# Kernel tuning notes

Measured on AMD Instinct MI355X. Metric: run time of the kernel, lower is better.

## Reference

```python
import jax, jax.numpy as jnp
import numpy as np

N_NODES = 100000


def gcn_conv(x, edge_index, edge_weight, W, b):
    """PyG GCNConv (normalize=True, add_self_loops=True): lin -> gcn_norm -> scatter-add -> +bias."""
    n = x.shape[0]
    src, dst = edge_index[0], edge_index[1]
    # add self-loops with fill_value=1
    loop = jnp.arange(n, dtype=edge_index.dtype)
    src = jnp.concatenate([src, loop])
    dst = jnp.concatenate([dst, loop])
    ew = jnp.concatenate([edge_weight, jnp.ones((n,), dtype=x.dtype)])
    # symmetric normalization: deg computed at target (col)
    deg = jax.ops.segment_sum(ew, dst, num_segments=n)
    dinv = jnp.where(deg > 0, jax.lax.rsqrt(deg), 0.0).astype(x.dtype)
    norm = dinv[src] * ew * dinv[dst]  # [E+N]
    xl = x @ W  # [N, out]
    msg = norm[:, None] * xl[src]  # gather + scale
    out = jax.ops.segment_sum(msg, dst, num_segments=n)  # scatter-add at target
    return out + b


def setup_inputs() -> dict:
    key = jax.random.key(0)
    ks = jax.random.split(key, 8)
    n, e = N_NODES, 1600000
    c_in, c_hid, c_out = 40, 64, 40
    x = jax.random.normal(ks[0], (n, c_in), dtype=jnp.float32)
    edge_index = jax.random.randint(ks[1], (2, e), 0, n, dtype=jnp.int64)
    edge_weight = jax.random.uniform(ks[2], (e,), dtype=jnp.float32)
    s1 = 1.0 / np.sqrt(c_in)
    s2 = 1.0 / np.sqrt(c_hid)
    W1 = jax.random.uniform(ks[3], (c_in, c_hid), dtype=jnp.float32, minval=-s1, maxval=s1)
    b1 = jnp.zeros((c_hid,), dtype=jnp.float32)
    W2 = jax.random.uniform(ks[4], (c_hid, c_out), dtype=jnp.float32, minval=-s2, maxval=s2)
    b2 = jnp.zeros((c_out,), dtype=jnp.float32)
    return {"x": x, "edge_index": edge_index, "edge_weight": edge_weight,
            "W1": W1, "b1": b1, "W2": W2, "b2": b2}


def reference(x, edge_index, edge_weight, W1, b1, W2, b2):
    # eval mode: dropout is identity
    h = gcn_conv(x, edge_index, edge_weight, W1, b1)
    h = jax.nn.relu(h)
    out = gcn_conv(h, edge_index, edge_weight, W2, b2)
    return out
```

## Files before the change

### kernel.cpp

```cpp
#include <hip/hip_runtime.h>
#include <hip/hip_fp16.h>

#define FIX 33554432.0f
#define FIXINV (1.0f / 33554432.0f)

typedef unsigned long long ull;

#define EB 1024
#define CSH 9
#define CNODES 512
#define MAXNB 256

__global__ void zero_small_k(int* p, int total) {
    int i = blockIdx.x * blockDim.x + threadIdx.x;
    if (i < total) p[i] = 0;
}

__global__ void bcount_k(const int* __restrict__ dst, int* __restrict__ bcnt, int e, int NB) {
    __shared__ int lh[MAXNB];
    for (int i = threadIdx.x; i < NB; i += blockDim.x) lh[i] = 0;
    __syncthreads();
    int cls = blockIdx.x & 7;
    int base = blockIdx.x * EB + threadIdx.x * 4;
    if (base + 3 < e) {
        int4 d4 = *reinterpret_cast<const int4*>(dst + base);
        atomicAdd(&lh[d4.x >> CSH], 1);
        atomicAdd(&lh[d4.y >> CSH], 1);
        atomicAdd(&lh[d4.z >> CSH], 1);
        atomicAdd(&lh[d4.w >> CSH], 1);
    } else {
        for (int i = base; i < e && i < base + 4; ++i) atomicAdd(&lh[dst[i] >> CSH], 1);
    }
    __syncthreads();
    for (int i = threadIdx.x; i < NB; i += blockDim.x) {
        int c = lh[i];
        if (c) atomicAdd(&bcnt[(i * 8 + cls) * 16], c);
    }
}

__global__ void bscan_k(const int* __restrict__ bcnt, int* __restrict__ bbase,
                        int* __restrict__ gcur, int M, int NB, int e) {
    __shared__ int lds[256];
    int per = (M + 255) / 256;
    int tid = threadIdx.x;
    int s = 0;
    for (int j = 0; j < per; ++j) {
        int idx = tid * per + j;
        if (idx < M) s += bcnt[idx * 16];
    }
    lds[tid] = s;
    __syncthreads();
    for (int off = 1; off < 256; off <<= 1) {
        int v = (tid >= off) ? lds[tid - off] : 0;
        __syncthreads();
        lds[tid] += v;
        __syncthreads();
    }
    int run = lds[tid] - s;
    for (int j = 0; j < per; ++j) {
        int idx = tid * per + j;
        if (idx < M) {
            gcur[idx * 16] = run;
            if ((idx & 7) == 0) bbase[idx >> 3] = run;
            run += bcnt[idx * 16];
        }
    }
    if (tid == 0) bbase[NB] = e;
}

__global__ void part1_k(const int* __restrict__ src, const int* __restrict__ dst,
                        const float* __restrict__ ew, int* gcur, ull* __restrict__ tmp,
                        int e, int NB) {
    __shared__ int lh[MAXNB];
    __shared__ int lb[MAXNB];
    for (int i = threadIdx.x; i < NB; i += blockDim.x) lh[i] = 0;
    __syncthreads();
    int cls = blockIdx.x & 7;
    int base = blockIdx.x * EB + threadIdx.x * 4;
    bool full = (blockIdx.x + 1) * EB <= e;
    int bk[4], ls[4];
    ull rec[4];
    bool val[4];
    if (full) {
        int4 s4 = *reinterpret_cast<const int4*>(src + base);
        int4 d4 = *reinterpret_cast<const int4*>(dst + base);
        float4 e4 = *reinterpret_cast<const float4*>(ew + base);
        int s[4] = {s4.x, s4.y, s4.z, s4.w};
        int d[4] = {d4.x, d4.y, d4.z, d4.w};
        float ev[4] = {e4.x, e4.y, e4.z, e4.w};
#pragma unroll
        for (int j = 0; j < 4; ++j) {
            val[j] = true;
            bk[j] = d[j] >> CSH;
            rec[j] = ((ull)__float_as_uint(ev[j]) << 26) | ((ull)(unsigned)s[j] << 9) |
                     (ull)(unsigned)(d[j] & (CNODES - 1));
            ls[j] = atomicAdd(&lh[bk[j]], 1);
        }
    } else {
#pragma unroll
        for (int j = 0; j < 4; ++j) {
            int i = base + j;
            val[j] = (i < e);
            int s = val[j] ? src[i] : 0;
            int d = val[j] ? dst[i] : 0;
            float ev = val[j] ? ew[i] : 0.0f;
            bk[j] = d >> CSH;
            rec[j] = ((ull)__float_as_uint(ev) << 26) | ((ull)(unsigned)s << 9) |
                     (ull)(unsigned)(d & (CNODES - 1));
            ls[j] = val[j] ? atomicAdd(&lh[bk[j]], 1) : 0;
        }
    }
    __syncthreads();
    for (int i = threadIdx.x; i < NB; i += blockDim.x) {
        int c = lh[i];
        lb[i] = c ? atomicAdd(&gcur[(i * 8 + cls) * 16], c) : 0;
    }
    __syncthreads();
#pragma unroll
    for (int j = 0; j < 4; ++j)
        if (val[j]) tmp[lb[bk[j]] + ls[j]] = rec[j];
}

__global__ __launch_bounds__(CNODES) void part2_k(const ull* __restrict__ tmp,
                                                  const int* __restrict__ bbase,
                                                  float* __restrict__ dinv,
                                                  int* __restrict__ rowptr,
                                                  uint2* __restrict__ csr,
                                                  int n, int e, int NB) {
    __shared__ ull ldc[CNODES];
    __shared__ int sc[CNODES];
    int b = blockIdx.x;
    int tid = threadIdx.x;
    ldc[tid] = 0;
    __syncthreads();
    int beg = bbase[b], end = bbase[b + 1];
    for (int i = beg + tid; i < end; i += CNODES) {
        ull rec = tmp[i];
        int dlo = (int)(rec & (CNODES - 1));
        float ewv = __uint_as_float((unsigned)(rec >> 26));
        atomicAdd(&ldc[dlo], (1ULL << 32) | (ull)__float2uint_rn(ewv * FIX));
    }
    __syncthreads();
    ull v = ldc[tid];
    int cnt = (int)(v >> 32);
    int node = b * CNODES + tid;
    if (node < n) {
        float d = (float)(unsigned)((unsigned)(v & 0xffffffffu) + (1u << 25)) * FIXINV;
        dinv[node] = rsqrtf(d);
    }
    sc[tid] = cnt;
    __syncthreads();
    for (int off = 1; off < CNODES; off <<= 1) {
        int x = (tid >= off) ? sc[tid - off] : 0;
        __syncthreads();
        sc[tid] += x;
        __syncthreads();
    }
    int slotbase = beg + sc[tid] - cnt;
    if (node < n) rowptr[node] = slotbase;
    if (b == NB - 1 && tid == 0) rowptr[n] = e;
    __syncthreads();
    sc[tid] = slotbase;
    __syncthreads();
    for (int i = beg + tid; i < end; i += CNODES) {
        ull rec = tmp[i];
        int dlo = (int)(rec & (CNODES - 1));
        unsigned s = (unsigned)((rec >> 9) & 0x1FFFF);
        unsigned ewb = (unsigned)(rec >> 26);
        int slot = atomicAdd(&sc[dlo], 1);
        csr[slot] = make_uint2(s, ewb);
    }
}

__global__ void tohalf_k(const float* __restrict__ x, const float* __restrict__ dinv,
                         __half* __restrict__ out, int n) {
    long gid = (long)blockIdx.x * blockDim.x + threadIdx.x;
    if (gid >= (long)n * 5) return;
    int row = (int)(gid / 5), c = (int)(gid % 5);
    float di = dinv[row];
    const float4* src = reinterpret_cast<const float4*>(x + (long)row * 40 + c * 8);
    float4 a = src[0], bb = src[1];
    __half2* dst = reinterpret_cast<__half2*>(out + (long)row * 40 + c * 8);
    dst[0] = __floats2half2_rn(di * a.x, di * a.y);
    dst[1] = __floats2half2_rn(di * a.z, di * a.w);
    dst[2] = __floats2half2_rn(di * bb.x, di * bb.y);
    dst[3] = __floats2half2_rn(di * bb.z, di * bb.w);
}

template <int K, int C, bool BIAS_RELU, bool DUAL16>
__global__ __launch_bounds__(256) void linear_k(const float* __restrict__ x,
                                                const float* __restrict__ W,
                                                const float* __restrict__ b,
                                                float* __restrict__ y,
                                                __half* __restrict__ y16,
                                                const float* __restrict__ dinv, int n) {
    int lane = threadIdx.x & 63;
    int wid = blockIdx.x * (blockDim.x >> 6) + (threadIdx.x >> 6);
    int nwaves = gridDim.x * (blockDim.x >> 6);
    float wreg[K];
#pragma unroll
    for (int k = 0; k < K; ++k) wreg[k] = (lane < C) ? W[k * C + lane] : 0.0f;
    float bias = (BIAS_RELU && lane < C) ? b[lane] : 0.0f;
    for (int node = wid; node < n; node += nwaves) {
        float xv = (lane < K) ? x[(long)node * K + lane] : 0.0f;
        unsigned xu = __float_as_uint(xv);
        float a0 = 0.0f, a1 = 0.0f, a2 = 0.0f, a3 = 0.0f;
#pragma unroll
        for (int k = 0; k < K; k += 4) {
            a0 = fmaf(__uint_as_float(__builtin_amdgcn_readlane(xu, k + 0)), wreg[k + 0], a0);
            a1 = fmaf(__uint_as_float(__builtin_amdgcn_readlane(xu, k + 1)), wreg[k + 1], a1);
            a2 = fmaf(__uint_as_float(__builtin_amdgcn_readlane(xu, k + 2)), wreg[k + 2], a2);
            a3 = fmaf(__uint_as_float(__builtin_amdgcn_readlane(xu, k + 3)), wreg[k + 3], a3);
        }
        float acc = (a0 + a1) + (a2 + a3);
        if (BIAS_RELU) acc = fmaxf(acc + bias, 0.0f);
        if (lane < C) {
            y[(long)node * C + lane] = acc;
            if (DUAL16) y16[(long)node * 40 + lane] = __float2half(dinv[node] * acc);
        }
    }
}

template <bool ADD_BIAS>
__global__ void gather40_k(const int* __restrict__ rowptr, const uint2* __restrict__ csr,
                           const __half* __restrict__ feat16, const float* __restrict__ selfF,
                           const float* __restrict__ dinv, const float* __restrict__ b,
                           float* __restrict__ out, int n) {
    int node = (int)(((long)blockIdx.x * blockDim.x + threadIdx.x) >> 6);
    int lane = threadIdx.x & 63;
    if (node >= n) return;
    int beg = __builtin_amdgcn_readfirstlane(rowptr[node]);
    int end = __builtin_amdgcn_readfirstlane(rowptr[node + 1]);
    if (lane >= 40) return;
    float accE = 0.0f;
    int t = beg;
    if (t < end && (t & 1)) {
        uint2 q = csr[t];
        accE = fmaf(__uint_as_float(q.y), __half2float(feat16[(long)q.x * 40 + lane]), accE);
        ++t;
    }
    for (; t + 7 < end; t += 8) {
        uint4 p0 = *reinterpret_cast<const uint4*>(csr + t);
        uint4 p1 = *reinterpret_cast<const uint4*>(csr + t + 2);
        uint4 p2 = *reinterpret_cast<const uint4*>(csr + t + 4);
        uint4 p3 = *reinterpret_cast<const uint4*>(csr + t + 6);
        float v0 = __half2float(feat16[(long)p0.x * 40 + lane]);
        float v1 = __half2float(feat16[(long)p0.z * 40 + lane]);
        float v2 = __half2float(feat16[(long)p1.x * 40 + lane]);
        float v3 = __half2float(feat16[(long)p1.z * 40 + lane]);
        float v4 = __half2float(feat16[(long)p2.x * 40 + lane]);
        float v5 = __half2float(feat16[(long)p2.z * 40 + lane]);
        float v6 = __half2float(feat16[(long)p3.x * 40 + lane]);
        float v7 = __half2float(feat16[(long)p3.z * 40 + lane]);
        accE = fmaf(__uint_as_float(p0.y), v0, accE);
        accE = fmaf(__uint_as_float(p0.w), v1, accE);
        accE = fmaf(__uint_as_float(p1.y), v2, accE);
        accE = fmaf(__uint_as_float(p1.w), v3, accE);
        accE = fmaf(__uint_as_float(p2.y), v4, accE);
        accE = fmaf(__uint_as_float(p2.w), v5, accE);
        accE = fmaf(__uint_as_float(p3.y), v6, accE);
        accE = fmaf(__uint_as_float(p3.w), v7, accE);
    }
    for (; t + 1 < end; t += 2) {
        uint4 p = *reinterpret_cast<const uint4*>(csr + t);
        float v0 = __half2float(feat16[(long)p.x * 40 + lane]);
        float v1 = __half2float(feat16[(long)p.z * 40 + lane]);
        accE = fmaf(__uint_as_float(p.y), v0, accE);
        accE = fmaf(__uint_as_float(p.w), v1, accE);
    }
    if (t < end) {
        uint2 q = csr[t];
        accE = fmaf(__uint_as_float(q.y), __half2float(feat16[(long)q.x * 40 + lane]), accE);
    }
    float di = dinv[node];
    float r = di * accE + di * di * selfF[(long)node * 40 + lane];
    if (ADD_BIAS) r += b[lane];
    out[(long)node * 40 + lane] = r;
}

extern "C" void kernel_launch(void* const* d_in, const int* in_sizes, int n_in,
                              void* d_out, int out_size, void* d_ws, size_t ws_size,
                              hipStream_t stream) {
    const float* x = (const float*)d_in[0];
    const int* ei = (const int*)d_in[1];
    const float* ew = (const float*)d_in[2];
    const float* W1 = (const float*)d_in[3];
    const float* b1 = (const float*)d_in[4];
    const float* W2 = (const float*)d_in[5];
    const float* b2 = (const float*)d_in[6];
    float* out = (float*)d_out;

    const int n = in_sizes[0] / 40;
    const int e = in_sizes[2];
    const int* srcp = ei;
    const int* dstp = ei + e;
    const int NB = (n + CNODES - 1) >> CSH;
    const int M = NB * 8;

    uint2* csr = (uint2*)d_ws;
    ull* tmp = (ull*)(((int*)d_ws) + 2 * (long)e);
    float* dinv = (float*)(tmp + e);
    int* rowptr = (int*)(dinv + n);
    int* bbase = rowptr + n + 1;
    int* bcnt = bbase + NB + 1;
    int* gcur = bcnt + M * 16;
    float* agg1 = (float*)(gcur + M * 16);
    float* h = agg1 + (long)n * 40;
    float* xl2_32 = agg1;
    __half* sh16 = (__half*)tmp;

    const int B = 256;
    auto cdiv = [](long a, long b) { return (int)((a + b - 1) / b); };
    const int egrid = cdiv(e, EB);

    zero_small_k<<<cdiv(M * 16, B), B, 0, stream>>>(bcnt, M * 16);
    bcount_k<<<egrid, B, 0, stream>>>(dstp, bcnt, e, NB);
    bscan_k<<<1, 256, 0, stream>>>(bcnt, bbase, gcur, M, NB, e);
    part1_k<<<egrid, B, 0, stream>>>(srcp, dstp, ew, gcur, tmp, e, NB);
    part2_k<<<NB, CNODES, 0, stream>>>(tmp, bbase, dinv, rowptr, csr, n, e, NB);

    tohalf_k<<<cdiv((long)n * 5, B), B, 0, stream>>>(x, dinv, sh16, n);

    gather40_k<false><<<cdiv((long)n * 64, B), B, 0, stream>>>(rowptr, csr, sh16, x, dinv, nullptr, agg1, n);
    linear_k<40, 64, true, false><<<2048, B, 0, stream>>>(agg1, W1, b1, h, nullptr, nullptr, n);

    linear_k<64, 40, false, true><<<2048, B, 0, stream>>>(h, W2, nullptr, xl2_32, sh16, dinv, n);
    gather40_k<true><<<cdiv((long)n * 64, B), B, 0, stream>>>(rowptr, csr, sh16, xl2_32, dinv, b2, out, n);
}
```

Before: 226.3 us.

## Fuse layer-1 gather with W1 linear and use half self-loop features

Merges the first-layer neighbor gather and the 40->64 linear+bias+ReLU into one persistent wave-per-node kernel, so the fp32 aggregate no longer makes a round trip through global memory. The self-loop term now reads the dinv-prescaled half features instead of fp32 inputs, which removes the fp32 xl2 store and the separate selfF read. The cost is lower precision on the self term, and the gather now runs with a grid-stride loop (4096 blocks) instead of one wave per node, which may reduce latency hiding.

```diff
diff --git a/kernel.cpp b/kernel.cpp
--- a/kernel.cpp
+++ b/kernel.cpp
@@ -187,56 +187,14 @@
     dst[3] = __floats2half2_rn(di * bb.z, di * bb.w);
 }
 
-template <int K, int C, bool BIAS_RELU, bool DUAL16>
-__global__ __launch_bounds__(256) void linear_k(const float* __restrict__ x,
-                                                const float* __restrict__ W,
-                                                const float* __restrict__ b,
-                                                float* __restrict__ y,
-                                                __half* __restrict__ y16,
-                                                const float* __restrict__ dinv, int n) {
-    int lane = threadIdx.x & 63;
-    int wid = blockIdx.x * (blockDim.x >> 6) + (threadIdx.x >> 6);
-    int nwaves = gridDim.x * (blockDim.x >> 6);
-    float wreg[K];
-#pragma unroll
-    for (int k = 0; k < K; ++k) wreg[k] = (lane < C) ? W[k * C + lane] : 0.0f;
-    float bias = (BIAS_RELU && lane < C) ? b[lane] : 0.0f;
-    for (int node = wid; node < n; node += nwaves) {
-        float xv = (lane < K) ? x[(long)node * K + lane] : 0.0f;
-        unsigned xu = __float_as_uint(xv);
-        float a0 = 0.0f, a1 = 0.0f, a2 = 0.0f, a3 = 0.0f;
-#pragma unroll
-        for (int k = 0; k < K; k += 4) {
-            a0 = fmaf(__uint_as_float(__builtin_amdgcn_readlane(xu, k + 0)), wreg[k + 0], a0);
-            a1 = fmaf(__uint_as_float(__builtin_amdgcn_readlane(xu, k + 1)), wreg[k + 1], a1);
-            a2 = fmaf(__uint_as_float(__builtin_amdgcn_readlane(xu, k + 2)), wreg[k + 2], a2);
-            a3 = fmaf(__uint_as_float(__builtin_amdgcn_readlane(xu, k + 3)), wreg[k + 3], a3);
-        }
-        float acc = (a0 + a1) + (a2 + a3);
-        if (BIAS_RELU) acc = fmaxf(acc + bias, 0.0f);
-        if (lane < C) {
-            y[(long)node * C + lane] = acc;
-            if (DUAL16) y16[(long)node * 40 + lane] = __float2half(dinv[node] * acc);
-        }
-    }
-}
-
-template <bool ADD_BIAS>
-__global__ void gather40_k(const int* __restrict__ rowptr, const uint2* __restrict__ csr,
-                           const __half* __restrict__ feat16, const float* __restrict__ selfF,
-                           const float* __restrict__ dinv, const float* __restrict__ b,
-                           float* __restrict__ out, int n) {
-    int node = (int)(((long)blockIdx.x * blockDim.x + threadIdx.x) >> 6);
-    int lane = threadIdx.x & 63;
-    if (node >= n) return;
-    int beg = __builtin_amdgcn_readfirstlane(rowptr[node]);
-    int end = __builtin_amdgcn_readfirstlane(rowptr[node + 1]);
-    if (lane >= 40) return;
+__device__ __forceinline__ float gather_core(const uint2* __restrict__ csr,
+                                             const __half* __restrict__ feat16,
+                                             int beg, int end, int ln) {
     float accE = 0.0f;
     int t = beg;
     if (t < end && (t & 1)) {
         uint2 q = csr[t];
-        accE = fmaf(__uint_as_float(q.y), __half2float(feat16[(long)q.x * 40 + lane]), accE);
+        accE = fmaf(__uint_as_float(q.y), __half2float(feat16[(long)q.x * 40 + ln]), accE);
         ++t;
     }
     for (; t + 7 < end; t += 8) {
@@ -244,14 +202,14 @@
         uint4 p1 = *reinterpret_cast<const uint4*>(csr + t + 2);
         uint4 p2 = *reinterpret_cast<const uint4*>(csr + t + 4);
         uint4 p3 = *reinterpret_cast<const uint4*>(csr + t + 6);
-        float v0 = __half2float(feat16[(long)p0.x * 40 + lane]);
-        float v1 = __half2float(feat16[(long)p0.z * 40 + lane]);
-        float v2 = __half2float(feat16[(long)p1.x * 40 + lane]);
-        float v3 = __half2float(feat16[(long)p1.z * 40 + lane]);
-        float v4 = __half2float(feat16[(long)p2.x * 40 + lane]);
-        float v5 = __half2float(feat16[(long)p2.z * 40 + lane]);
-        float v6 = __half2float(feat16[(long)p3.x * 40 + lane]);
-        float v7 = __half2float(feat16[(long)p3.z * 40 + lane]);
+        float v0 = __half2float(feat16[(long)p0.x * 40 + ln]);
+        float v1 = __half2float(feat16[(long)p0.z * 40 + ln]);
+        float v2 = __half2float(feat16[(long)p1.x * 40 + ln]);
+        float v3 = __half2float(feat16[(long)p1.z * 40 + ln]);
+        float v4 = __half2float(feat16[(long)p2.x * 40 + ln]);
+        float v5 = __half2float(feat16[(long)p2.z * 40 + ln]);
+        float v6 = __half2float(feat16[(long)p3.x * 40 + ln]);
+        float v7 = __half2float(feat16[(long)p3.z * 40 + ln]);
         accE = fmaf(__uint_as_float(p0.y), v0, accE);
         accE = fmaf(__uint_as_float(p0.w), v1, accE);
         accE = fmaf(__uint_as_float(p1.y), v2, accE);
@@ -263,19 +221,92 @@
     }
     for (; t + 1 < end; t += 2) {
         uint4 p = *reinterpret_cast<const uint4*>(csr + t);
-        float v0 = __half2float(feat16[(long)p.x * 40 + lane]);
-        float v1 = __half2float(feat16[(long)p.z * 40 + lane]);
+        float v0 = __half2float(feat16[(long)p.x * 40 + ln]);
+        float v1 = __half2float(feat16[(long)p.z * 40 + ln]);
         accE = fmaf(__uint_as_float(p.y), v0, accE);
         accE = fmaf(__uint_as_float(p.w), v1, accE);
     }
     if (t < end) {
         uint2 q = csr[t];
-        accE = fmaf(__uint_as_float(q.y), __half2float(feat16[(long)q.x * 40 + lane]), accE);
-    }
+        accE = fmaf(__uint_as_float(q.y), __half2float(feat16[(long)q.x * 40 + ln]), accE);
+    }
+    return accE;
+}
+
+__global__ __launch_bounds__(256) void gatherlin_k(const int* __restrict__ rowptr,
+                                                   const uint2* __restrict__ csr,
+                                                   const __half* __restrict__ feat16,
+                                                   const float* __restrict__ dinv,
+                                                   const float* __restrict__ W1,
+                                                   const float* __restrict__ b1,
+                                                   float* __restrict__ h, int n) {
+    int lane = threadIdx.x & 63;
+    int wid = blockIdx.x * (blockDim.x >> 6) + (threadIdx.x >> 6);
+    int nwaves = gridDim.x * (blockDim.x >> 6);
+    float w1reg[40];
+#pragma unroll
+    for (int k = 0; k < 40; ++k) w1reg[k] = W1[k * 64 + lane];
+    float b1v = b1[lane];
+    int ln = (lane < 40) ? lane : 0;
+    for (int node = wid; node < n; node += nwaves) {
+        int beg = __builtin_amdgcn_readfirstlane(rowptr[node]);
+        int end = __builtin_amdgcn_readfirstlane(rowptr[node + 1]);
+        float accE = gather_core(csr, feat16, beg, end, ln);
+        float selfv = __half2float(feat16[(long)node * 40 + ln]);
+        float di = dinv[node];
+        unsigned aggu = __float_as_uint(di * (accE + selfv));
+        float a0 = 0.0f, a1 = 0.0f, a2 = 0.0f, a3 = 0.0f;
+#pragma unroll
+        for (int k = 0; k < 40; k += 4) {
+            a0 = fmaf(__uint_as_float(__builtin_amdgcn_readlane(aggu, k + 0)), w1reg[k + 0], a0);
+            a1 = fmaf(__uint_as_float(__builtin_amdgcn_readlane(aggu, k + 1)), w1reg[k + 1], a1);
+            a2 = fmaf(__uint_as_float(__builtin_amdgcn_readlane(aggu, k + 2)), w1reg[k + 2], a2);
+            a3 = fmaf(__uint_as_float(__builtin_amdgcn_readlane(aggu, k + 3)), w1reg[k + 3], a3);
+        }
+        float hv = fmaxf((a0 + a1) + (a2 + a3) + b1v, 0.0f);
+        h[(long)node * 64 + lane] = hv;
+    }
+}
+
+__global__ __launch_bounds__(256) void linear2_k(const float* __restrict__ h,
+                                                 const float* __restrict__ W2,
+                                                 __half* __restrict__ y16,
+                                                 const float* __restrict__ dinv, int n) {
+    int lane = threadIdx.x & 63;
+    int wid = blockIdx.x * (blockDim.x >> 6) + (threadIdx.x >> 6);
+    int nwaves = gridDim.x * (blockDim.x >> 6);
+    float wreg[64];
+#pragma unroll
+    for (int k = 0; k < 64; ++k) wreg[k] = (lane < 40) ? W2[k * 40 + lane] : 0.0f;
+    for (int node = wid; node < n; node += nwaves) {
+        float xv = h[(long)node * 64 + lane];
+        unsigned xu = __float_as_uint(xv);
+        float a0 = 0.0f, a1 = 0.0f, a2 = 0.0f, a3 = 0.0f;
+#pragma unroll
+        for (int k = 0; k < 64; k += 4) {
+            a0 = fmaf(__uint_as_float(__builtin_amdgcn_readlane(xu, k + 0)), wreg[k + 0], a0);
+            a1 = fmaf(__uint_as_float(__builtin_amdgcn_readlane(xu, k + 1)), wreg[k + 1], a1);
+            a2 = fmaf(__uint_as_float(__builtin_amdgcn_readlane(xu, k + 2)), wreg[k + 2], a2);
+            a3 = fmaf(__uint_as_float(__builtin_amdgcn_readlane(xu, k + 3)), wreg[k + 3], a3);
+        }
+        float acc = (a0 + a1) + (a2 + a3);
+        if (lane < 40) y16[(long)node * 40 + lane] = __float2half(dinv[node] * acc);
+    }
+}
+
+__global__ void gather40_k(const int* __restrict__ rowptr, const uint2* __restrict__ csr,
+                           const __half* __restrict__ feat16, const float* __restrict__ dinv,
+                           const float* __restrict__ b, float* __restrict__ out, int n) {
+    int node = (int)(((long)blockIdx.x * blockDim.x + threadIdx.x) >> 6);
+    int lane = threadIdx.x & 63;
+    if (node >= n) return;
+    int beg = __builtin_amdgcn_readfirstlane(rowptr[node]);
+    int end = __builtin_amdgcn_readfirstlane(rowptr[node + 1]);
+    if (lane >= 40) return;
+    float accE = gather_core(csr, feat16, beg, end, lane);
+    float selfv = __half2float(feat16[(long)node * 40 + lane]);
     float di = dinv[node];
-    float r = di * accE + di * di * selfF[(long)node * 40 + lane];
-    if (ADD_BIAS) r += b[lane];
-    out[(long)node * 40 + lane] = r;
+    out[(long)node * 40 + lane] = di * (accE + selfv) + b[lane];
 }
 
 extern "C" void kernel_launch(void* const* d_in, const int* in_sizes, int n_in,
@@ -304,9 +335,8 @@
     int* bbase = rowptr + n + 1;
     int* bcnt = bbase + NB + 1;
     int* gcur = bcnt + M * 16;
-    float* agg1 = (float*)(gcur + M * 16);
-    float* h = agg1 + (long)n * 40;
-    float* xl2_32 = agg1;
+    float* h = (float*)(gcur + M * 16);
+    __half* xl2_16 = (__half*)(h + (long)n * 64);
     __half* sh16 = (__half*)tmp;
 
     const int B = 256;
@@ -321,9 +351,8 @@
 
     tohalf_k<<<cdiv((long)n * 5, B), B, 0, stream>>>(x, dinv, sh16, n);
 
-    gather40_k<false><<<cdiv((long)n * 64, B), B, 0, stream>>>(rowptr, csr, sh16, x, dinv, nullptr, agg1, n);
-    linear_k<40, 64, true, false><<<2048, B, 0, stream>>>(agg1, W1, b1, h, nullptr, nullptr, n);
-
-    linear_k<64, 40, false, true><<<2048, B, 0, stream>>>(h, W2, nullptr, xl2_32, sh16, dinv, n);
-    gather40_k<true><<<cdiv((long)n * 64, B), B, 0, stream>>>(rowptr, csr, sh16, xl2_32, dinv, b2, out, n);
-}
+    gatherlin_k<<<4096, B, 0, stream>>>(rowptr, csr, sh16, dinv, W1, b1, h, n);
+
+    linear2_k<<<2048, B, 0, stream>>>(h, W2, xl2_16, dinv, n);
+    gather40_k<<<cdiv((long)n * 64, B), B, 0, stream>>>(rowptr, csr, xl2_16, dinv, b2, out, n);
+}
```

Result: faster. 218.5 us (-3.5%).
